# Optimization experiments

Measured on AMD Instinct MI355X. Metric: run time of the kernel, lower is better.

## Reference

```python
import jax, jax.numpy as jnp
import numpy as np
from jax import lax

C, S, Q = 20, 8, 16          # n_class, n_support, n_query
IMW, IMH, CH = 84, 84, 3     # image width, height, channels
CNT = 17.0                   # 1 aug + 8 same-class + 8 adversarial pair terms (loop break logic with S=8)

def _conv(x, k, b):
    return lax.conv_general_dilated(x, k, (1, 1), 'SAME',
                                    dimension_numbers=('NHWC', 'HWIO', 'NHWC')) + b

def _pool(x):
    return lax.reduce_window(x, -jnp.inf, lax.max, (1, 2, 2, 1), (1, 2, 2, 1), 'VALID')

def _d2(a, b):
    # calc_euclidian_dists: MEAN of squared differences over feature dim
    return jnp.mean((a - b) ** 2, axis=-1)

def _encoder(x, p):
    (k1, b1, k2, b2, k3, b3, k4, b4, k5, b5, k6, b6, k7, b7, k8, b8,
     g1, be1, g2, be2) = p
    x = _conv(x, k1, b1); x = _conv(x, k2, b2); x = _conv(x, k3, b3); x = _conv(x, k4, b4)
    x = _pool(jax.nn.relu(g1 * x + be1))
    x = _conv(x, k5, b5); x = _conv(x, k6, b6); x = _conv(x, k7, b7); x = _conv(x, k8, b8)
    x = _pool(jax.nn.relu(g2 * x + be2))
    return x.reshape(x.shape[0], -1)

def _pro_encoder(x, p, Wm):
    # same layers, each layer output scaled by W[i] (the `self.W[i] * layer` intent)
    (k1, b1, k2, b2, k3, b3, k4, b4, k5, b5, k6, b6, k7, b7, k8, b8,
     g1, be1, g2, be2) = p
    x = Wm[0] * _conv(x, k1, b1); x = Wm[1] * _conv(x, k2, b2)
    x = Wm[2] * _conv(x, k3, b3); x = Wm[3] * _conv(x, k4, b4)
    x = Wm[4] * (g1 * x + be1); x = Wm[5] * jax.nn.relu(x); x = Wm[6] * _pool(x)
    x = Wm[7] * _conv(x, k5, b5); x = Wm[8] * _conv(x, k6, b6)
    x = Wm[9] * _conv(x, k7, b7); x = Wm[10] * _conv(x, k8, b8)
    x = Wm[11] * (g2 * x + be2); x = Wm[12] * jax.nn.relu(x); x = Wm[13] * _pool(x)
    return Wm[14] * x.reshape(x.shape[0], -1)

def setup_inputs():
    key = jax.random.key(0)
    ks = jax.random.split(key, 24)
    def kern(k, cin):
        return jax.random.normal(k, (3, 3, cin, 16), jnp.float32) * 0.05
    inp = {
        'support': jax.random.normal(ks[0], (C, S, IMW, IMH, CH), jnp.float32),
        'query':   jax.random.normal(ks[1], (C, Q, IMW, IMH, CH), jnp.float32),
        'k1': kern(ks[2], CH)}
    for i in range(2, 9):
        inp['k%d' % i] = kern(ks[1 + i], 16)
    for i in range(1, 9):
        inp['b%d' % i] = jax.random.normal(ks[9 + i], (16,), jnp.float32) * 0.01
    inp['g1'] = jnp.ones((16,), jnp.float32)
    inp['be1'] = jnp.zeros((16,), jnp.float32)
    inp['g2'] = jnp.ones((16,), jnp.float32)
    inp['be2'] = jnp.zeros((16,), jnp.float32)
    inp['Wm'] = jax.random.normal(ks[20], (19,), jnp.float32)
    return inp

def _forward(support, query, p, Wm):
    n_class, n_support = support.shape[0], support.shape[1]
    n_query = query.shape[1]
    cat = jnp.concatenate([support.reshape(-1, IMW, IMH, CH),
                           query.reshape(-1, IMW, IMH, CH)], axis=0)
    z = _encoder(cat, p)
    D = z.shape[-1]
    z1 = z[:n_class * n_support].reshape(n_class, n_support, D)
    # tf.image.flip_left_right flips the second-to-last (width) axis of each image
    z_aug = _encoder(jnp.flip(support, axis=-2).reshape(-1, IMW, IMH, CH), p)
    z_aug = z_aug.reshape(n_class, n_support, D)
    d_aug = _d2(z1, z_aug) ** 2                                       # [C,S]
    # same-class pairwise terms: with S=8 the loop adds all 8 supports then breaks
    pos = jnp.sum(_d2(z1[:, :, None, :], z1[:, None, :, :]) ** 2, axis=2)
    z_adv = jnp.roll(z1, -1, axis=0)                                  # adversarial class (c+1)%C
    neg = jnp.sum(_d2(z1[:, :, None, :], z_adv[:, None, :, :]) ** 2, axis=2)
    uns_loss = jnp.sum((d_aug + pos - neg) / CNT + 0.5)
    zp = _pro_encoder(cat, p, Wm)
    protos = zp[:n_class * n_support].reshape(n_class, n_support, D).mean(axis=1)
    zq = zp[n_class * n_support:]
    dists = _d2(zq[:, None, :], protos[None, :, :])                   # [C*Q, C]
    log_p = jax.nn.log_softmax(-dists, axis=-1).reshape(n_class, n_query, n_class)
    y = jnp.tile(jnp.arange(n_class)[:, None], (1, n_query))
    ce = -jnp.mean(jnp.take_along_axis(log_p, y[:, :, None], axis=-1))
    loss = ce + uns_loss
    acc = jnp.mean((jnp.argmax(log_p, axis=-1) == y).astype(jnp.float32))
    return loss, acc

def reference(support, query, k1, k2, k3, k4, k5, k6, k7, k8,
              b1, b2, b3, b4, b5, b6, b7, b8, g1, be1, g2, be2, Wm):
    p = (k1, b1, k2, b2, k3, b3, k4, b4, k5, b5, k6, b6, k7, b7, k8, b8,
         g1, be1, g2, be2)
    return _forward(support, query, p, Wm)
```

## Files before the change

### kernel.cpp

```cpp
#include <hip/hip_runtime.h>
#include <math.h>


typedef __attribute__((ext_vector_type(8))) short bf16x8;
typedef __attribute__((ext_vector_type(8))) unsigned short u16x8;
typedef __attribute__((ext_vector_type(4))) float f32x4;
typedef unsigned short u16;
typedef unsigned int u32;

#define PIX84 (84 * 84)
#define D     (21 * 21 * 16)
#define WF_LAYER 3072
#define WF_C1 (7 * WF_LAYER)

__device__ __forceinline__ float bf2f(u16 v) {
    union { u32 i; float f; } c; c.i = ((u32)v) << 16; return c.f;
}
__device__ __forceinline__ u16 f2bf(float f) {
    union { float f; u32 i; } c; c.f = f;
    u32 r = c.i + 0x7fffu + ((c.i >> 16) & 1u);
    return (u16)(r >> 16);
}
__device__ __forceinline__ u32 pack2(float a, float b) {
    union { __bf16 h[2]; u32 u; } p;
    p.h[0] = (__bf16)a; p.h[1] = (__bf16)b;
    return p.u;
}

__device__ __forceinline__ bf16x8 ld_bf16x8_a8(const char* p) {
    union { uint2 q[2]; bf16x8 v; } u;
    u.q[0] = *(const uint2*)(p);
    u.q[1] = *(const uint2*)(p + 8);
    return u.v;
}

__device__ __forceinline__ float blockReduceSum(float v) {
    __shared__ float red[8];
    #pragma unroll
    for (int o = 32; o > 0; o >>= 1) v += __shfl_down(v, o, 64);
    const int lane = threadIdx.x & 63, wid = threadIdx.x >> 6;
    __syncthreads();
    if (lane == 0) red[wid] = v;
    __syncthreads();
    float r = 0.f;
    if (threadIdx.x == 0) {
        const int nw = (blockDim.x + 63) >> 6;
        for (int i = 0; i < nw; ++i) r += red[i];
    }
    return r;
}

__global__ void prep_weights(const float* __restrict__ k1, const float* __restrict__ k2,
                             const float* __restrict__ k3, const float* __restrict__ k4,
                             const float* __restrict__ k5, const float* __restrict__ k6,
                             const float* __restrict__ k7, const float* __restrict__ k8,
                             u16* __restrict__ wf)
{
    const int idx = blockIdx.x * 256 + threadIdx.x;
    if (idx < WF_C1) {
        const int j = idx & 7, lane = (idx >> 3) & 63, r = idx >> 9;
        const int s = r % 6, L = r / 6;
        const float* ks[7] = { k2, k3, k4, k5, k6, k7, k8 };
        const int co = lane & 15, g = lane >> 4;
        const int k = g * 8 + j;
        const int t = k >> 4, ci = k & 15;
        float v = 0.f;
        if (t == 0)      v = ks[L][(s * 16 + ci) * 16 + co];
        else if (s >= 3) v = ks[L][((s + 3) * 16 + ci) * 16 + co];
        wf[idx] = f2bf(v);
    } else if (idx < WF_C1 + 1024) {
        const int t = idx - WF_C1;
        const int j = t & 7, lane = (t >> 3) & 63, m = t >> 9;
        const int co = lane & 15, g = lane >> 4;
        const int k = g * 8 + j;
        const int dh  = (m == 0) ? (k >> 4) : 2;
        const int rem = (m == 0) ? (k & 15) : k;
        const int dw = rem >> 2, ci = rem & 3;
        const float v = (rem < 12 && ci < 3) ? k1[((dh * 3 + dw) * 3 + ci) * 16 + co] : 0.f;
        wf[idx] = f2bf(v);
    }
}

template <int W, int LW, int MAXT, int HALF>
__device__ __forceinline__ void conv_layer(char* buf, const u16* wfL,
                                           const float* bias, float scale,
                                           int nrows, int dro, int lane, int wv)
{
    const int g = lane >> 4, col = lane & 15;
    bf16x8 wfr[6];
    #pragma unroll
    for (int s = 0; s < 6; ++s) wfr[s] = ((const bf16x8*)wfL)[s * 64 + lane];
    const float4 bv = *(const float4*)(bias + g * 4);
    const float c0 = bv.x * scale, c1 = bv.y * scale;
    const float c2 = bv.z * scale, c3 = bv.w * scale;
    const int NPX = nrows * W;
    const int TC = (NPX + 15) >> 4;
    const int t0 = wv * MAXT;
    const int rb_const = (g & 1) * HALF + (g >> 1) * (LW * 16);
    const int wb_const = (g >> 1) * HALF + (g & 1) * 8 + (dro * LW + 1) * 16;

    f32x4 acc[MAXT];
    #pragma unroll
    for (int u = 0; u < MAXT; ++u) {
        const int t = t0 + u;
        if (t < TC) {
            const int px = t * 16 + col;
            const int p = (px < NPX) ? px : 0;
            const int j = p / W, w = p - j * W;
            const char* rb = buf + rb_const + (j * LW + w) * 16;
            f32x4 a = { 0.f, 0.f, 0.f, 0.f };
            a = __builtin_amdgcn_mfma_f32_16x16x32_bf16(wfr[0], *(const bf16x8*)(rb),                a, 0, 0, 0);
            a = __builtin_amdgcn_mfma_f32_16x16x32_bf16(wfr[1], *(const bf16x8*)(rb + 16),           a, 0, 0, 0);
            a = __builtin_amdgcn_mfma_f32_16x16x32_bf16(wfr[2], *(const bf16x8*)(rb + 32),           a, 0, 0, 0);
            a = __builtin_amdgcn_mfma_f32_16x16x32_bf16(wfr[3], *(const bf16x8*)(rb + LW * 16),      a, 0, 0, 0);
            a = __builtin_amdgcn_mfma_f32_16x16x32_bf16(wfr[4], *(const bf16x8*)(rb + LW * 16 + 16), a, 0, 0, 0);
            a = __builtin_amdgcn_mfma_f32_16x16x32_bf16(wfr[5], *(const bf16x8*)(rb + LW * 16 + 32), a, 0, 0, 0);
            acc[u] = a;
        }
    }
    __syncthreads();
    #pragma unroll
    for (int u = 0; u < MAXT; ++u) {
        const int t = t0 + u;
        if (t < TC) {
            const int px = t * 16 + col;
            if (px < NPX) {
                const int j = px / W, w = px - j * W;
                const u32 lo = pack2(fmaf(acc[u][0], scale, c0), fmaf(acc[u][1], scale, c1));
                const u32 hi = pack2(fmaf(acc[u][2], scale, c2), fmaf(acc[u][3], scale, c3));
                *(uint2*)(buf + wb_const + (j * LW + w) * 16) = make_uint2(lo, hi);
            }
        }
    }
    __syncthreads();
}

#define NP1   (20 * 86)
#define HALF1 (NP1 * 16)
__global__ __launch_bounds__(512) void stage1_kernel(
    const float* __restrict__ sup, const float* __restrict__ qry,
    const float* __restrict__ b1,
    const u16* __restrict__ wf,
    const float* __restrict__ b2, const float* __restrict__ b3,
    const float* __restrict__ b4,
    const float* __restrict__ g1, const float* __restrict__ be1,
    const float* __restrict__ Wm,
    u16* __restrict__ s1out)
{
    __shared__ char buf[2 * HALF1];
    __shared__ u16 stag[(22 * 86 + 2) * 4];
    const int img = blockIdx.x / 6, bb = blockIdx.x % 6;
    const int R0 = 14 * bb;
    const int tid = threadIdx.x, lane = tid & 63, wv = tid >> 6;
    const bool pro = img >= 320;

    const float* src;
    bool flip = false;
    if (img < 160) src = sup + (size_t)img * (PIX84 * 3);
    else if (img < 320) { src = sup + (size_t)(img - 160) * (PIX84 * 3); flip = true; }
    else {
        const int m = img - 320;
        src = (m < 160) ? sup + (size_t)m * (PIX84 * 3)
                        : qry + (size_t)(m - 160) * (PIX84 * 3);
    }
    const float s1 = pro ? Wm[0] : 1.f, s2 = pro ? Wm[1] : 1.f;
    const float s3 = pro ? Wm[2] : 1.f, s4 = pro ? Wm[3] : 1.f;
    const float pre = pro ? Wm[4] : 1.f, rs = pro ? Wm[5] : 1.f;
    const float post = pro ? Wm[6] : 1.f;

    for (int i = tid; i < 40; i += 512) {
        const int P = (i >> 1) * 86 + ((i & 1) ? 85 : 0);
        *(uint4*)(buf + P * 16) = make_uint4(0, 0, 0, 0);
        *(uint4*)(buf + HALF1 + P * 16) = make_uint4(0, 0, 0, 0);
    }

    for (int p = tid; p < 22 * 86; p += 512) {
        const int r = p / 86, c = p - r * 86;
        const int hin = R0 - 4 + r, win = c - 1;
        u32 lo = 0, hi = 0;
        if ((unsigned)hin < 84u && (unsigned)win < 84u) {
            const int wsrc = flip ? (83 - win) : win;
            const float* ip = src + ((size_t)(hin * 84 + wsrc)) * 3;
            lo = pack2(ip[0], ip[1]);
            hi = pack2(ip[2], 0.f);
        }
        *(uint2*)((char*)stag + (size_t)p * 8) = make_uint2(lo, hi);
    }
    __syncthreads();

    {
        const int g = lane >> 4, col = lane & 15;
        const bf16x8 wA0 = ((const bf16x8*)(wf + WF_C1))[lane];
        const bf16x8 wA1 = ((const bf16x8*)(wf + WF_C1))[64 + lane];
        const float4 bv = *(const float4*)(b1 + g * 4);
        const int off0 = ((g >> 1) * 86 + (g & 1) * 2) * 8;
        const int off1 = (2 * 86 + (g & 1) * 2) * 8;
        const int wb_const = (g >> 1) * HALF1 + (g & 1) * 8;
        for (int t = wv; t < 105; t += 8) {
            const int p = t * 16 + col;
            const int ri = p / 84, w = p - ri * 84;
            const int base = (ri * 86 + w) * 8;
            const bf16x8 B0 = ld_bf16x8_a8((const char*)stag + base + off0);
            const bf16x8 B1 = ld_bf16x8_a8((const char*)stag + base + off1);
            f32x4 a = { 0.f, 0.f, 0.f, 0.f };
            a = __builtin_amdgcn_mfma_f32_16x16x32_bf16(wA0, B0, a, 0, 0, 0);
            a = __builtin_amdgcn_mfma_f32_16x16x32_bf16(wA1, B1, a, 0, 0, 0);
            const int h = R0 - 3 + ri;
            const float sc = ((unsigned)h < 84u) ? s1 : 0.f;
            const u32 lo = pack2((a[0] + bv.x) * sc, (a[1] + bv.y) * sc);
            const u32 hi = pack2((a[2] + bv.z) * sc, (a[3] + bv.w) * sc);
            *(uint2*)(buf + wb_const + (ri * 86 + (w + 1)) * 16) = make_uint2(lo, hi);
        }
    }
    __syncthreads();

    conv_layer<84, 86, 12, HALF1>(buf, wf,                b2, s2, 18, 0, lane, wv);
    conv_layer<84, 86, 11, HALF1>(buf, wf + WF_LAYER,     b3, s3, 16, 0, lane, wv);
    conv_layer<84, 86, 10, HALF1>(buf, wf + 2 * WF_LAYER, b4, s4, 14, 0, lane, wv);

    for (int e = tid; e < 7 * 42 * 2; e += 512) {
        const int hf = e & 1;
        const int pc = (e >> 1) % 42, pr = (e >> 1) / 42;
        float mx[8];
        #pragma unroll
        for (int c = 0; c < 8; ++c) mx[c] = -1e30f;
        #pragma unroll
        for (int dy = 0; dy < 2; ++dy)
            #pragma unroll
            for (int dx = 0; dx < 2; ++dx) {
                const int P = (2 * pr + dy) * 86 + (2 * pc + dx + 1);
                const u16x8 vv = *(const u16x8*)(buf + hf * HALF1 + P * 16);
                #pragma unroll
                for (int c = 0; c < 8; ++c) {
                    const int ch = hf * 8 + c;
                    const float t =
                        rs * fmaxf(0.f, pre * fmaf(g1[ch], bf2f(vv[c]), be1[ch]));
                    mx[c] = fmaxf(mx[c], t);
                }
            }
        uint4 o;
        o.x = pack2(post * mx[0], post * mx[1]);
        o.y = pack2(post * mx[2], post * mx[3]);
        o.z = pack2(post * mx[4], post * mx[5]);
        o.w = pack2(post * mx[6], post * mx[7]);
        *(uint4*)(s1out + (size_t)img * 28224 +
                  ((size_t)(7 * bb + pr) * 42 + pc) * 16 + hf * 8) = o;
    }
}

#define NP2   (44 * 44)
#define HALF2 (NP2 * 16)
__global__ __launch_bounds__(512) void stage2_kernel(
    const u16* __restrict__ s1in, const u16* __restrict__ wf,
    const float* __restrict__ b5, const float* __restrict__ b6,
    const float* __restrict__ b7, const float* __restrict__ b8,
    const float* __restrict__ g2, const float* __restrict__ be2,
    const float* __restrict__ Wm,
    float* __restrict__ z, float* __restrict__ zp)
{
    __shared__ char buf[2 * HALF2];
    const int img = blockIdx.x;
    const int tid = threadIdx.x, lane = tid & 63, wv = tid >> 6;
    const bool pro = img >= 320;
    const float s5 = pro ? Wm[7] : 1.f, s6 = pro ? Wm[8] : 1.f;
    const float s7 = pro ? Wm[9] : 1.f, s8 = pro ? Wm[10] : 1.f;
    const float pre = pro ? Wm[11] : 1.f, rs = pro ? Wm[12] : 1.f;
    const float post = pro ? (Wm[13] * Wm[14]) : 1.f;

    for (int i = tid; i < 44 * 44; i += 512) {
        const int r = i / 44, c = i - r * 44;
        if (r == 0 || r == 43 || c == 0 || c == 43) {
            *(uint4*)(buf + i * 16) = make_uint4(0, 0, 0, 0);
            *(uint4*)(buf + HALF2 + i * 16) = make_uint4(0, 0, 0, 0);
        }
    }
    const u16* ip = s1in + (size_t)img * 28224;
    for (int cix = tid; cix < 42 * 42 * 2; cix += 512) {
        const int Pi = cix >> 1, hf = cix & 1;
        const int r = Pi / 42, c = Pi - r * 42;
        const uint4 v = *(const uint4*)(ip + (size_t)cix * 8);
        *(uint4*)(buf + hf * HALF2 + ((r + 1) * 44 + (c + 1)) * 16) = v;
    }
    __syncthreads();

    conv_layer<42, 44, 14, HALF2>(buf, wf + 3 * WF_LAYER, b5, s5, 42, 1, lane, wv);
    conv_layer<42, 44, 14, HALF2>(buf, wf + 4 * WF_LAYER, b6, s6, 42, 1, lane, wv);
    conv_layer<42, 44, 14, HALF2>(buf, wf + 5 * WF_LAYER, b7, s7, 42, 1, lane, wv);
    conv_layer<42, 44, 14, HALF2>(buf, wf + 6 * WF_LAYER, b8, s8, 42, 1, lane, wv);

    float* outp = pro ? (zp + (size_t)(img - 320) * D) : (z + (size_t)img * D);
    for (int e = tid; e < 21 * 21 * 2; e += 512) {
        const int hf = e & 1;
        const int pc = (e >> 1) % 21, pr = (e >> 1) / 21;
        float mx[8];
        #pragma unroll
        for (int c = 0; c < 8; ++c) mx[c] = -1e30f;
        #pragma unroll
        for (int dy = 0; dy < 2; ++dy)
            #pragma unroll
            for (int dx = 0; dx < 2; ++dx) {
                const int P = (2 * pr + dy + 1) * 44 + (2 * pc + dx + 1);
                const u16x8 vv = *(const u16x8*)(buf + hf * HALF2 + P * 16);
                #pragma unroll
                for (int c = 0; c < 8; ++c) {
                    const int ch = hf * 8 + c;
                    const float t =
                        rs * fmaxf(0.f, pre * fmaf(g2[ch], bf2f(vv[c]), be2[ch]));
                    mx[c] = fmaxf(mx[c], t);
                }
            }
        float* op = outp + ((size_t)(pr * 21 + pc)) * 16 + hf * 8;
        float4 o0 = make_float4(post * mx[0], post * mx[1], post * mx[2], post * mx[3]);
        float4 o1 = make_float4(post * mx[4], post * mx[5], post * mx[6], post * mx[7]);
        *(float4*)op = o0;
        *(float4*)(op + 4) = o1;
    }
}

__global__ void pairs_kernel(const float* __restrict__ z,
                             float* __restrict__ within, float* __restrict__ cross,
                             float* __restrict__ aug)
{
    const int bid = blockIdx.x;
    const float *u, *v;
    float* dst;
    if (bid < 1280) {
        const int c = bid / 64, i = (bid % 64) / 8, j = bid % 8;
        u = z + (size_t)(c * 8 + i) * D;
        v = z + (size_t)(c * 8 + j) * D;
        dst = within + bid;
    } else if (bid < 2560) {
        const int t = bid - 1280;
        const int c = t / 64, i = (t % 64) / 8, j = t % 8;
        const int c2 = (c + 1) % 20;
        u = z + (size_t)(c * 8 + i) * D;
        v = z + (size_t)(c2 * 8 + j) * D;
        dst = cross + t;
    } else {
        const int t = bid - 2560;
        u = z + (size_t)t * D;
        v = z + (size_t)(160 + t) * D;
        dst = aug + t;
    }
    const float4* u4 = (const float4*)u;
    const float4* v4 = (const float4*)v;
    float s = 0.f;
    for (int d = threadIdx.x; d < D / 4; d += 256) {
        const float4 a = u4[d], b = v4[d];
        const float dx = a.x - b.x, dy = a.y - b.y, dz = a.z - b.z, dw = a.w - b.w;
        s += dx * dx + dy * dy + dz * dz + dw * dw;
    }
    s = blockReduceSum(s);
    if (threadIdx.x == 0) {
        const float m = s / (float)D;
        *dst = m * m;
    }
}

__global__ void protos_kernel(const float* __restrict__ zp, float* __restrict__ protos)
{
    const int idx = blockIdx.x * 256 + threadIdx.x;
    if (idx >= 20 * D) return;
    const int c = idx / D, d = idx % D;
    float s = 0.f;
    #pragma unroll
    for (int i = 0; i < 8; ++i) s += zp[(size_t)(c * 8 + i) * D + d];
    protos[idx] = s * 0.125f;
}

__global__ void dists_kernel(const float* __restrict__ zq, const float* __restrict__ protos,
                             float* __restrict__ dists)
{
    const int q = blockIdx.x / 20, c = blockIdx.x % 20;
    const float4* u4 = (const float4*)(zq + (size_t)q * D);
    const float4* v4 = (const float4*)(protos + (size_t)c * D);
    float s = 0.f;
    for (int d = threadIdx.x; d < D / 4; d += 256) {
        const float4 a = u4[d], b = v4[d];
        const float dx = a.x - b.x, dy = a.y - b.y, dz = a.z - b.z, dw = a.w - b.w;
        s += dx * dx + dy * dy + dz * dz + dw * dw;
    }
    s = blockReduceSum(s);
    if (threadIdx.x == 0) dists[blockIdx.x] = s / (float)D;
}

__global__ void final_kernel(const float* __restrict__ dists,
                             const float* __restrict__ within,
                             const float* __restrict__ cross,
                             const float* __restrict__ aug,
                             float* __restrict__ out)
{
    float ce = 0.f, accv = 0.f, uns = 0.f;
    for (int r = threadIdx.x; r < 320; r += 256) {
        const float* dr = dists + r * 20;
        const int y = r / 16;
        float dmin = dr[0];
        int amin = 0;
        float m = -dr[0];
        #pragma unroll
        for (int j = 1; j < 20; ++j) {
            if (dr[j] < dmin) { dmin = dr[j]; amin = j; }
            m = fmaxf(m, -dr[j]);
        }
        float se = 0.f;
        #pragma unroll
        for (int j = 0; j < 20; ++j) se += expf(-dr[j] - m);
        const float lse = m + logf(se);
        ce += dr[y] + lse;
        accv += (amin == y) ? 1.0f : 0.0f;
    }
    for (int i = threadIdx.x; i < 1280; i += 256) uns += within[i] - cross[i];
    for (int i = threadIdx.x; i < 160; i += 256) uns += aug[i];

    ce = blockReduceSum(ce);
    accv = blockReduceSum(accv);
    uns = blockReduceSum(uns);
    if (threadIdx.x == 0) {
        out[0] = ce / 320.0f + uns / 17.0f + 80.0f;
        out[1] = accv / 320.0f;
    }
}

extern "C" void kernel_launch(void* const* d_in, const int* in_sizes, int n_in,
                              void* d_out, int out_size, void* d_ws, size_t ws_size,
                              hipStream_t stream)
{
    (void)in_sizes; (void)n_in; (void)out_size; (void)ws_size;
    const float* sup = (const float*)d_in[0];
    const float* qry = (const float*)d_in[1];
    const float* K[8]; for (int i = 0; i < 8; ++i) K[i] = (const float*)d_in[2 + i];
    const float* B[8]; for (int i = 0; i < 8; ++i) B[i] = (const float*)d_in[10 + i];
    const float* g1  = (const float*)d_in[18];
    const float* be1 = (const float*)d_in[19];
    const float* g2  = (const float*)d_in[20];
    const float* be2 = (const float*)d_in[21];
    const float* Wm  = (const float*)d_in[22];
    float* out = (float*)d_out;

    size_t off = 0;
    auto alloc = [&](size_t bytes) -> void* {
        void* p = (char*)d_ws + off;
        off += (bytes + 255) & ~(size_t)255;
        return p;
    };
    u16*   wf     = (u16*)alloc((size_t)(WF_C1 + 1024) * 2);
    u16*   s1out  = (u16*)alloc((size_t)800 * 42 * 42 * 16 * 2);
    float* z      = (float*)alloc((size_t)320 * D * 4);
    float* zp     = (float*)alloc((size_t)480 * D * 4);
    float* within = (float*)alloc(1280 * 4);
    float* crossb = (float*)alloc(1280 * 4);
    float* augb   = (float*)alloc(160 * 4);
    float* protos = (float*)alloc((size_t)20 * D * 4);
    float* dist   = (float*)alloc(6400 * 4);

    prep_weights<<<(WF_C1 + 1024 + 255) / 256, 256, 0, stream>>>(
        K[0], K[1], K[2], K[3], K[4], K[5], K[6], K[7], wf);

    stage1_kernel<<<800 * 6, 512, 0, stream>>>(sup, qry, B[0], wf,
                                               B[1], B[2], B[3], g1, be1, Wm, s1out);
    stage2_kernel<<<800, 512, 0, stream>>>(s1out, wf, B[4], B[5], B[6], B[7],
                                           g2, be2, Wm, z, zp);

    pairs_kernel<<<2720, 256, 0, stream>>>(z, within, crossb, augb);
    protos_kernel<<<(20 * D + 255) / 256, 256, 0, stream>>>(zp, protos);
    dists_kernel<<<6400, 256, 0, stream>>>(zp + (size_t)160 * D, protos, dist);
    final_kernel<<<1, 256, 0, stream>>>(dist, within, crossb, augb, out);
}
```

Baseline: 292.0 us.

## Pad LDS row strides to avoid bank conflicts and simplify pooling epilogue

```diff
diff --git a/kernel.cpp b/kernel.cpp
--- a/kernel.cpp
+++ b/kernel.cpp
@@ -97,9 +97,10 @@
     const int TC = (NPX + 15) >> 4;
     const int t0 = wv * MAXT;
     const int rb_const = (g & 1) * HALF + (g >> 1) * (LW * 16);
-    const int wb_const = (g >> 1) * HALF + (g & 1) * 8 + (dro * LW + 1) * 16;
+    const int w2r = ((g >> 1) * HALF + (g & 1) * 8 + (dro * LW + 1) * 16) - rb_const;
 
     f32x4 acc[MAXT];
+    int raddr[MAXT];
     #pragma unroll
     for (int u = 0; u < MAXT; ++u) {
         const int t = t0 + u;
@@ -107,7 +108,9 @@
             const int px = t * 16 + col;
             const int p = (px < NPX) ? px : 0;
             const int j = p / W, w = p - j * W;
-            const char* rb = buf + rb_const + (j * LW + w) * 16;
+            const int ra = rb_const + (j * LW + w) * 16;
+            raddr[u] = ra;
+            const char* rb = buf + ra;
             f32x4 a = { 0.f, 0.f, 0.f, 0.f };
             a = __builtin_amdgcn_mfma_f32_16x16x32_bf16(wfr[0], *(const bf16x8*)(rb),                a, 0, 0, 0);
             a = __builtin_amdgcn_mfma_f32_16x16x32_bf16(wfr[1], *(const bf16x8*)(rb + 16),           a, 0, 0, 0);
@@ -125,18 +128,16 @@
         if (t < TC) {
             const int px = t * 16 + col;
             if (px < NPX) {
-                const int j = px / W, w = px - j * W;
                 const u32 lo = pack2(fmaf(acc[u][0], scale, c0), fmaf(acc[u][1], scale, c1));
                 const u32 hi = pack2(fmaf(acc[u][2], scale, c2), fmaf(acc[u][3], scale, c3));
-                *(uint2*)(buf + wb_const + (j * LW + w) * 16) = make_uint2(lo, hi);
+                *(uint2*)(buf + raddr[u] + w2r) = make_uint2(lo, hi);
             }
         }
     }
     __syncthreads();
 }
 
-#define NP1   (20 * 86)
-#define HALF1 (NP1 * 16)
+#define HALF1 (20 * 86 * 16 + 16)
 __global__ __launch_bounds__(512) void stage1_kernel(
     const float* __restrict__ sup, const float* __restrict__ qry,
     const float* __restrict__ b1,
@@ -218,38 +219,42 @@
     conv_layer<84, 86, 11, HALF1>(buf, wf + WF_LAYER,     b3, s3, 16, 0, lane, wv);
     conv_layer<84, 86, 10, HALF1>(buf, wf + 2 * WF_LAYER, b4, s4, 14, 0, lane, wv);
 
+    const u32 uPRS = __float_as_uint(pre * rs);
+    const float AR = post * rs;
     for (int e = tid; e < 7 * 42 * 2; e += 512) {
         const int hf = e & 1;
         const int pc = (e >> 1) % 42, pr = (e >> 1) / 42;
-        float mx[8];
+        const char* hb = buf + hf * HALF1;
+        const int P0 = (2 * pr) * 86 + (2 * pc + 1);
+        const u16x8 v00 = *(const u16x8*)(hb + P0 * 16);
+        const u16x8 v01 = *(const u16x8*)(hb + (P0 + 1) * 16);
+        const u16x8 v10 = *(const u16x8*)(hb + (P0 + 86) * 16);
+        const u16x8 v11 = *(const u16x8*)(hb + (P0 + 87) * 16);
+        float o[8];
         #pragma unroll
-        for (int c = 0; c < 8; ++c) mx[c] = -1e30f;
-        #pragma unroll
-        for (int dy = 0; dy < 2; ++dy)
-            #pragma unroll
-            for (int dx = 0; dx < 2; ++dx) {
-                const int P = (2 * pr + dy) * 86 + (2 * pc + dx + 1);
-                const u16x8 vv = *(const u16x8*)(buf + hf * HALF1 + P * 16);
-                #pragma unroll
-                for (int c = 0; c < 8; ++c) {
-                    const int ch = hf * 8 + c;
-                    const float t =
-                        rs * fmaxf(0.f, pre * fmaf(g1[ch], bf2f(vv[c]), be1[ch]));
-                    mx[c] = fmaxf(mx[c], t);
-                }
-            }
-        uint4 o;
-        o.x = pack2(post * mx[0], post * mx[1]);
-        o.y = pack2(post * mx[2], post * mx[3]);
-        o.z = pack2(post * mx[4], post * mx[5]);
-        o.w = pack2(post * mx[6], post * mx[7]);
+        for (int c = 0; c < 8; ++c) {
+            const int ch = hf * 8 + c;
+            const float x0 = bf2f(v00[c]), x1 = bf2f(v01[c]);
+            const float x2 = bf2f(v10[c]), x3 = bf2f(v11[c]);
+            const float mx = fmaxf(fmaxf(fmaxf(x0, x1), x2), x3);
+            const float mn = fminf(fminf(fminf(x0, x1), x2), x3);
+            const float gch = g1[ch];
+            const bool dn = ((__float_as_uint(gch) ^ uPRS) >> 31) != 0;
+            const float m = dn ? mn : mx;
+            o[c] = AR * fmaxf(0.f, fmaf(pre * gch, m, pre * be1[ch]));
+        }
+        uint4 ov;
+        ov.x = pack2(o[0], o[1]);
+        ov.y = pack2(o[2], o[3]);
+        ov.z = pack2(o[4], o[5]);
+        ov.w = pack2(o[6], o[7]);
         *(uint4*)(s1out + (size_t)img * 28224 +
-                  ((size_t)(7 * bb + pr) * 42 + pc) * 16 + hf * 8) = o;
-    }
-}
-
-#define NP2   (44 * 44)
-#define HALF2 (NP2 * 16)
+                  ((size_t)(7 * bb + pr) * 42 + pc) * 16 + hf * 8) = ov;
+    }
+}
+
+#define LW2   46
+#define HALF2 (44 * LW2 * 16 + 16)
 __global__ __launch_bounds__(512) void stage2_kernel(
     const u16* __restrict__ s1in, const u16* __restrict__ wf,
     const float* __restrict__ b5, const float* __restrict__ b6,
@@ -270,8 +275,9 @@
     for (int i = tid; i < 44 * 44; i += 512) {
         const int r = i / 44, c = i - r * 44;
         if (r == 0 || r == 43 || c == 0 || c == 43) {
-            *(uint4*)(buf + i * 16) = make_uint4(0, 0, 0, 0);
-            *(uint4*)(buf + HALF2 + i * 16) = make_uint4(0, 0, 0, 0);
+            const int P = r * LW2 + c;
+            *(uint4*)(buf + P * 16) = make_uint4(0, 0, 0, 0);
+            *(uint4*)(buf + HALF2 + P * 16) = make_uint4(0, 0, 0, 0);
         }
     }
     const u16* ip = s1in + (size_t)img * 28224;
@@ -279,41 +285,43 @@
         const int Pi = cix >> 1, hf = cix & 1;
         const int r = Pi / 42, c = Pi - r * 42;
         const uint4 v = *(const uint4*)(ip + (size_t)cix * 8);
-        *(uint4*)(buf + hf * HALF2 + ((r + 1) * 44 + (c + 1)) * 16) = v;
-    }
-    __syncthreads();
-
-    conv_layer<42, 44, 14, HALF2>(buf, wf + 3 * WF_LAYER, b5, s5, 42, 1, lane, wv);
-    conv_layer<42, 44, 14, HALF2>(buf, wf + 4 * WF_LAYER, b6, s6, 42, 1, lane, wv);
-    conv_layer<42, 44, 14, HALF2>(buf, wf + 5 * WF_LAYER, b7, s7, 42, 1, lane, wv);
-    conv_layer<42, 44, 14, HALF2>(buf, wf + 6 * WF_LAYER, b8, s8, 42, 1, lane, wv);
+        *(uint4*)(buf + hf * HALF2 + ((r + 1) * LW2 + (c + 1)) * 16) = v;
+    }
+    __syncthreads();
+
+    conv_layer<42, LW2, 14, HALF2>(buf, wf + 3 * WF_LAYER, b5, s5, 42, 1, lane, wv);
+    conv_layer<42, LW2, 14, HALF2>(buf, wf + 4 * WF_LAYER, b6, s6, 42, 1, lane, wv);
+    conv_layer<42, LW2, 14, HALF2>(buf, wf + 5 * WF_LAYER, b7, s7, 42, 1, lane, wv);
+    conv_layer<42, LW2, 14, HALF2>(buf, wf + 6 * WF_LAYER, b8, s8, 42, 1, lane, wv);
 
     float* outp = pro ? (zp + (size_t)(img - 320) * D) : (z + (size_t)img * D);
+    const u32 uPRS = __float_as_uint(pre * rs);
+    const float AR = post * rs;
     for (int e = tid; e < 21 * 21 * 2; e += 512) {
         const int hf = e & 1;
         const int pc = (e >> 1) % 21, pr = (e >> 1) / 21;
-        float mx[8];
+        const char* hb = buf + hf * HALF2;
+        const int P0 = (2 * pr + 1) * LW2 + (2 * pc + 1);
+        const u16x8 v00 = *(const u16x8*)(hb + P0 * 16);
+        const u16x8 v01 = *(const u16x8*)(hb + (P0 + 1) * 16);
+        const u16x8 v10 = *(const u16x8*)(hb + (P0 + LW2) * 16);
+        const u16x8 v11 = *(const u16x8*)(hb + (P0 + LW2 + 1) * 16);
+        float o[8];
         #pragma unroll
-        for (int c = 0; c < 8; ++c) mx[c] = -1e30f;
-        #pragma unroll
-        for (int dy = 0; dy < 2; ++dy)
-            #pragma unroll
-            for (int dx = 0; dx < 2; ++dx) {
-                const int P = (2 * pr + dy + 1) * 44 + (2 * pc + dx + 1);
-                const u16x8 vv = *(const u16x8*)(buf + hf * HALF2 + P * 16);
-                #pragma unroll
-                for (int c = 0; c < 8; ++c) {
-                    const int ch = hf * 8 + c;
-                    const float t =
-                        rs * fmaxf(0.f, pre * fmaf(g2[ch], bf2f(vv[c]), be2[ch]));
-                    mx[c] = fmaxf(mx[c], t);
-                }
-            }
+        for (int c = 0; c < 8; ++c) {
+            const int ch = hf * 8 + c;
+            const float x0 = bf2f(v00[c]), x1 = bf2f(v01[c]);
+            const float x2 = bf2f(v10[c]), x3 = bf2f(v11[c]);
+            const float mx = fmaxf(fmaxf(fmaxf(x0, x1), x2), x3);
+            const float mn = fminf(fminf(fminf(x0, x1), x2), x3);
+            const float gch = g2[ch];
+            const bool dn = ((__float_as_uint(gch) ^ uPRS) >> 31) != 0;
+            const float m = dn ? mn : mx;
+            o[c] = AR * fmaxf(0.f, fmaf(pre * gch, m, pre * be2[ch]));
+        }
         float* op = outp + ((size_t)(pr * 21 + pc)) * 16 + hf * 8;
-        float4 o0 = make_float4(post * mx[0], post * mx[1], post * mx[2], post * mx[3]);
-        float4 o1 = make_float4(post * mx[4], post * mx[5], post * mx[6], post * mx[7]);
-        *(float4*)op = o0;
-        *(float4*)(op + 4) = o1;
+        *(float4*)op = make_float4(o[0], o[1], o[2], o[3]);
+        *(float4*)(op + 4) = make_float4(o[4], o[5], o[6], o[7]);
     }
 }
 
```

Measured after the change: 295.3 us. No clear change (+1.1%).
